# Kernel optimization log

Hardware: AMD Instinct MI355X
Metric: run time of the kernel (lower is better)

The kernel has to match this reference:

```python
import jax, jax.numpy as jnp
import numpy as np

K = 3  # inferred kernel size (28->26->pool->13->11->pool->5 matches 32*5*5 FC input)


def _patches(x, k=K):
    # x: (N,C,H,W) -> (N,C,k*k,OH,OW) valid patches, stride 1
    N, C, H, W = x.shape
    OH, OW = H - k + 1, W - k + 1
    return jnp.stack(
        [x[:, :, i:i + OH, j:j + OW] for i in range(k) for j in range(k)], axis=2
    )


def _maxpool2(x):
    N, C, H, W = x.shape
    H2, W2 = H // 2, W // 2
    x = x[:, :, :H2 * 2, :W2 * 2].reshape(N, C, H2, 2, W2, 2)
    return x.max(axis=(3, 5))


def _lc2d(x, w, b):
    # unshared-weight locally connected conv: w (O,C,k*k,OH,OW), b (O,OH,OW)
    p = _patches(x)  # (N,C,k*k,OH,OW)
    return jnp.einsum('nckij,ockij->noij', p, w) + b


def setup_inputs():
    key = jax.random.key(0)
    ks = jax.random.split(key, 9)
    s = 0.05
    return {
        'x': jax.random.normal(ks[0], (4096, 1, 28, 28), jnp.float32),
        'w1': jax.random.normal(ks[1], (16, 1, 9, 26, 26), jnp.float32) * s,
        'b1': jax.random.normal(ks[2], (16, 26, 26), jnp.float32) * s,
        'w2': jax.random.normal(ks[3], (32, 16, 9, 11, 11), jnp.float32) * s,
        'b2': jax.random.normal(ks[4], (32, 11, 11), jnp.float32) * s,
        'fc1_w': jax.random.normal(ks[5], (32 * 5 * 5, 128), jnp.float32) * s,
        'fc1_b': jax.random.normal(ks[6], (128,), jnp.float32) * s,
        'fc2_w': jax.random.normal(ks[7], (128, 10), jnp.float32) * s,
        'fc2_b': jax.random.normal(ks[8], (10,), jnp.float32) * s,
    }


def reference(x, w1, b1, w2, b2, fc1_w, fc1_b, fc2_w, fc2_b):
    h = _maxpool2(jax.nn.relu(_lc2d(x, w1, b1)))      # (N,16,13,13)
    h = _maxpool2(jax.nn.relu(_lc2d(h, w2, b2)))      # (N,32,5,5)
    h = h.reshape(h.shape[0], -1)                      # (N,800)
    h = jax.nn.relu(h @ fc1_w + fc1_b)                 # (N,128)
    return h @ fc2_w + fc2_b                           # (N,10)
```

## Files before the change

kernel.cpp:

```cpp
#include <hip/hip_runtime.h>

#define NB 4096

typedef __attribute__((ext_vector_type(8))) short s8v;
typedef __attribute__((ext_vector_type(4))) float f4v;

#define XB_OFF  0u
#define H1B_OFF 6422528u
#define H2B_OFF 28573696u
#define W2B_OFF 35127296u
#define B2R_OFF 36765696u
#define W1B_OFF 36778496u
#define B1R_OFF 37470720u
#define WFB_OFF 37513984u

__device__ __forceinline__ unsigned short f2bf(float f) {
  unsigned int u = __builtin_bit_cast(unsigned int, f);
  u += 0x7fffu + ((u >> 16) & 1u);
  return (unsigned short)(u >> 16);
}

__global__ __launch_bounds__(256) void k_prep(const float* __restrict__ x,
                                              const float* __restrict__ w1,
                                              const float* __restrict__ b1,
                                              const float* __restrict__ w2,
                                              const float* __restrict__ b2,
                                              const float* __restrict__ f1w,
                                              short* __restrict__ xB,
                                              short* __restrict__ w1b,
                                              float* __restrict__ b1r,
                                              short* __restrict__ w2b,
                                              float* __restrict__ b2r,
                                              short* __restrict__ wfb) {
  const int bx = blockIdx.x;
  if (bx < 1600) {
    __shared__ float t2[64][33];
    const int c0 = (bx % 25) * 32;
    const int n0 = (bx / 25) * 64;
    const int tx = threadIdx.x & 31, ty = threadIdx.x >> 5;
    const int c = c0 + tx;
    #pragma unroll
    for (int i = 0; i < 64; i += 8)
      if (c < 784) t2[ty + i][tx] = x[(n0 + ty + i) * 784 + c];
    __syncthreads();
    const int cl = threadIdx.x >> 3;
    const int ns = (threadIdx.x & 7) * 8;
    if (c0 + cl < 784) {
      unsigned short v[8];
      #pragma unroll
      for (int q = 0; q < 8; q++) v[q] = f2bf(t2[ns + q][cl]);
      *reinterpret_cast<s8v*>(&xB[(c0 + cl) * NB + n0 + ns]) =
          *reinterpret_cast<const s8v*>(v);
    }
  } else if (bx < 1769) {
    const int q = (bx - 1600) * 256 + threadIdx.x;
    const int l = q & 63;
    const int cv = (q >> 6) & 3;
    const int pos = q >> 8;
    const int o = l & 15;
    const int i = pos / 13, j = pos % 13;
    const int dy = cv >> 1, dx = cv & 1;
    unsigned short v[8];
    #pragma unroll
    for (int t = 0; t < 8; t++) {
      const int k = (l >> 4) * 8 + t;
      float f = 0.f;
      if (k < 16) {
        const int py = k >> 2, px = k & 3;
        const int ky = py - dy, kx = px - dx;
        if (ky >= 0 && ky < 3 && kx >= 0 && kx < 3)
          f = w1[(o * 9 + ky * 3 + kx) * 676 + (2 * i + dy) * 26 + 2 * j + dx];
      }
      v[t] = f2bf(f);
    }
    *reinterpret_cast<s8v*>(&w1b[q * 8]) = *reinterpret_cast<const s8v*>(v);
  } else if (bx < 1812) {
    const int idx = (bx - 1769) * 256 + threadIdx.x;
    if (idx < 10816) {
      const int cv = idx & 3;
      const int o = (idx >> 2) & 15;
      const int pos = idx >> 6;
      const int i = pos / 13, j = pos % 13;
      b1r[idx] = b1[(o * 26 + 2 * i + (cv >> 1)) * 26 + 2 * j + (cv & 1)];
    }
  } else if (bx < 2212) {
    const int q = (bx - 1812) * 256 + threadIdx.x;
    const int l = q & 63;
    const int ot = (q >> 6) & 1;
    const int s = (q >> 7) & 7;
    const int cv = (q >> 10) & 3;
    const int pos = q >> 12;
    const int o = ot * 16 + (l & 15);
    const int dy = cv >> 1, dx = cv & 1;
    const int I = pos / 5, J = pos % 5;
    unsigned short v[8];
    #pragma unroll
    for (int t = 0; t < 8; t++) {
      const int k = s * 32 + (l >> 4) * 8 + t;
      const int w = k >> 4, c = k & 15;
      const int py = w >> 2, px = w & 3;
      const int ky = py - dy, kx = px - dx;
      float f = 0.f;
      if (ky >= 0 && ky < 3 && kx >= 0 && kx < 3)
        f = w2[((o * 16 + c) * 9 + ky * 3 + kx) * 121 +
               (2 * I + dy) * 11 + (2 * J + dx)];
      v[t] = f2bf(f);
    }
    *reinterpret_cast<s8v*>(&w2b[q * 8]) = *reinterpret_cast<const s8v*>(v);
  } else if (bx == 2212) {
    for (int q = threadIdx.x; q < 3200; q += 256) {
      const int pos = q >> 7;
      const int r = q & 127;
      const int o = r >> 2, cv = r & 3;
      const int I = pos / 5, J = pos % 5;
      b2r[q] = b2[o * 121 + (2 * I + (cv >> 1)) * 11 + 2 * J + (cv & 1)];
    }
  } else {
    const int q = (bx - 2213) * 256 + threadIdx.x;
    const int l = q & 63;
    const int jt = (q >> 6) & 7;
    const int s = q >> 9;
    const int j = jt * 16 + (l & 15);
    unsigned short v[8];
    #pragma unroll
    for (int t = 0; t < 8; t++) {
      const int o = (l >> 4) * 8 + t;
      v[t] = f2bf(f1w[(o * 25 + s) * 128 + j]);
    }
    *reinterpret_cast<s8v*>(&wfb[q * 8]) = *reinterpret_cast<const s8v*>(v);
  }
}

__global__ __launch_bounds__(256, 3) void k_lc1(const short* __restrict__ xB,
                                                const short* __restrict__ w1b,
                                                const float* __restrict__ b1r,
                                                short* __restrict__ h1b) {
  __shared__ short sx[16 * 264 + 16 + 8];
  __shared__ unsigned short ush[256 * 24];
  const int pos = blockIdx.y;
  const int i = pos / 13, j = pos % 13;
  const int tid = threadIdx.x;
  const int l = tid & 63;
  const int wv = tid >> 6;
  const int lm = l & 15, kg = l >> 4;
  const int n0b = blockIdx.x * 256;

  #pragma unroll
  for (int rr = 0; rr < 2; rr++) {
    const int idx = rr * 256 + tid;
    const int row = idx >> 5, seg = idx & 31;
    const int grow = (2 * i + (row >> 2)) * 28 + (2 * j + (row & 3));
    *reinterpret_cast<s8v*>(&sx[row * 264 + ((row >> 3) & 1) * 16 + seg * 8]) =
        *reinterpret_cast<const s8v*>(&xB[grow * NB + n0b + seg * 8]);
  }

  s8v bf[4];
  #pragma unroll
  for (int cv = 0; cv < 4; cv++)
    bf[cv] = *reinterpret_cast<const s8v*>(w1b + ((pos * 4 + cv) * 64 + l) * 8);
  const float4 bias = *reinterpret_cast<const float4*>(b1r + (pos * 16 + lm) * 4);
  __syncthreads();

  f4v acc[4][4];
  #pragma unroll
  for (int a = 0; a < 4; a++)
    #pragma unroll
    for (int cv = 0; cv < 4; cv++) acc[a][cv] = (f4v){0.f, 0.f, 0.f, 0.f};

  #pragma unroll
  for (int a = 0; a < 4; a++) {
    const int nl = wv * 64 + a * 16 + lm;
    s8v av = (s8v){0, 0, 0, 0, 0, 0, 0, 0};
    if (kg < 2) {
      #pragma unroll
      for (int t = 0; t < 8; t++) {
        const int k = kg * 8 + t;
        av[t] = sx[k * 264 + ((k >> 3) & 1) * 16 + nl];
      }
    }
    #pragma unroll
    for (int cv = 0; cv < 4; cv++)
      acc[a][cv] =
          __builtin_amdgcn_mfma_f32_16x16x32_bf16(av, bf[cv], acc[a][cv], 0, 0, 0);
  }

  #pragma unroll
  for (int a = 0; a < 4; a++) {
    #pragma unroll
    for (int reg = 0; reg < 4; reg++) {
      const int nl = wv * 64 + a * 16 + kg * 4 + reg;
      const float v =
          fmaxf(fmaxf(acc[a][0][reg] + bias.x, acc[a][1][reg] + bias.y),
                fmaxf(acc[a][2][reg] + bias.z, acc[a][3][reg] + bias.w));
      ush[nl * 24 + lm] = f2bf(fmaxf(v, 0.f));
    }
  }
  __syncthreads();

  short* dst = h1b + (pos * 4096 + n0b + tid) * 16;
  const unsigned short* src = ush + tid * 24;
  *reinterpret_cast<s8v*>(dst) = *reinterpret_cast<const s8v*>(src);
  *reinterpret_cast<s8v*>(dst + 8) = *reinterpret_cast<const s8v*>(src + 8);
}

__global__ __launch_bounds__(256, 2) void k_lc2(const short* __restrict__ h1b,
                                                const short* __restrict__ w2b,
                                                const float* __restrict__ b2r,
                                                short* __restrict__ h2b) {
  __shared__ short sb[32768];
  const int pos = blockIdx.y;
  const int I = pos / 5, J = pos % 5;
  const int tid = threadIdx.x;
  const int l = tid & 63;
  const int wave = tid >> 6;
  const int wm = wave >> 1, ot = wave & 1;
  const int nw = blockIdx.x * 128 + wm * 64;
  const int kg = l >> 4;
  const int lm = l & 15;
  const int c0 = (kg & 1) * 8;
  const int whalf = kg >> 1;

  const short* wsrc = w2b + pos * 32768;
  #pragma unroll
  for (int r = 0; r < 16; r++) {
    const int idx = r * 256 + tid;
    *reinterpret_cast<s8v*>(&sb[idx * 8]) =
        *reinterpret_cast<const s8v*>(&wsrc[idx * 8]);
  }
  __syncthreads();

  f4v acc[4][4];
  #pragma unroll
  for (int a = 0; a < 4; a++)
    #pragma unroll
    for (int cv = 0; cv < 4; cv++)
      acc[a][cv] = (f4v){0.f, 0.f, 0.f, 0.f};

  #pragma unroll
  for (int s = 0; s < 8; s++) {
    const int wdw = s * 2 + whalf;
    const int py = wdw >> 2, px = wdw & 3;
    const int p = (2 * I + py) * 13 + (2 * J + px);
    const int abase = (p * 4096 + nw + lm) * 16 + c0;
    s8v av[4];
    #pragma unroll
    for (int a = 0; a < 4; a++)
      av[a] = *reinterpret_cast<const s8v*>(h1b + abase + a * 256);
    #pragma unroll
    for (int cv = 0; cv < 4; cv++) {
      const s8v bf = *reinterpret_cast<const s8v*>(
          &sb[(((cv * 8 + s) * 2 + ot) * 64 + l) * 8]);
      #pragma unroll
      for (int a = 0; a < 4; a++)
        acc[a][cv] =
            __builtin_amdgcn_mfma_f32_16x16x32_bf16(av[a], bf, acc[a][cv], 0, 0, 0);
    }
  }

  const int o = ot * 16 + lm;
  const float4 bias = *reinterpret_cast<const float4*>(b2r + (pos * 32 + o) * 4);
  #pragma unroll
  for (int a = 0; a < 4; a++) {
    const int nb = nw + a * 16 + kg * 4;
    #pragma unroll
    for (int reg = 0; reg < 4; reg++) {
      const float v =
          fmaxf(fmaxf(acc[a][0][reg] + bias.x, acc[a][1][reg] + bias.y),
                fmaxf(acc[a][2][reg] + bias.z, acc[a][3][reg] + bias.w));
      h2b[(pos * 4096 + nb + reg) * 32 + o] = (short)f2bf(fmaxf(v, 0.f));
    }
  }
}

__global__ __launch_bounds__(256) void k_fc(const short* __restrict__ h2b,
                                            const short* __restrict__ wfb,
                                            const float* __restrict__ f1b,
                                            const float* __restrict__ f2w,
                                            const float* __restrict__ f2b,
                                            float* __restrict__ out) {
  __shared__ float sh3[128 * 17];
  __shared__ float swf2[128 * 12];
  __shared__ float sb1[128];
  const int tid = threadIdx.x;
  const int l = tid & 63;
  const int w = tid >> 6;
  const int lm = l & 15, kg = l >> 4;
  const int n0 = blockIdx.x * 16;
  const int jt0 = w * 2;

  for (int idx = tid; idx < 1536; idx += 256) {
    const int kk = idx / 12, f = idx % 12;
    swf2[idx] = (f < 10) ? f2w[kk * 10 + f] : 0.f;
  }
  if (tid < 128) sb1[tid] = f1b[tid];

  f4v acc0 = (f4v){0.f, 0.f, 0.f, 0.f};
  f4v acc1 = (f4v){0.f, 0.f, 0.f, 0.f};

  #pragma unroll
  for (int s = 0; s < 25; s++) {
    const s8v av = *reinterpret_cast<const s8v*>(
        h2b + (s * 4096 + n0 + lm) * 32 + kg * 8);
    const s8v b0 = *reinterpret_cast<const s8v*>(
        wfb + ((s * 8 + jt0) * 64 + l) * 8);
    const s8v b1v = *reinterpret_cast<const s8v*>(
        wfb + ((s * 8 + jt0 + 1) * 64 + l) * 8);
    acc0 = __builtin_amdgcn_mfma_f32_16x16x32_bf16(av, b0, acc0, 0, 0, 0);
    acc1 = __builtin_amdgcn_mfma_f32_16x16x32_bf16(av, b1v, acc1, 0, 0, 0);
  }
  __syncthreads();

  #pragma unroll
  for (int q = 0; q < 2; q++) {
    const f4v a = q ? acc1 : acc0;
    const int j = (jt0 + q) * 16 + lm;
    #pragma unroll
    for (int reg = 0; reg < 4; reg++)
      sh3[j * 17 + kg * 4 + reg] = fmaxf(a[reg] + sb1[j], 0.f);
  }
  __syncthreads();

  if (tid < 160) {
    const int oo = tid >> 4, nn = tid & 15;
    float s = f2b[oo];
    for (int j = 0; j < 128; j++)
      s += sh3[j * 17 + nn] * swf2[j * 12 + oo];
    out[(n0 + nn) * 10 + oo] = s;
  }
}

extern "C" void kernel_launch(void* const* d_in, const int* in_sizes, int n_in,
                              void* d_out, int out_size, void* d_ws,
                              size_t ws_size, hipStream_t stream) {
  const float* x   = (const float*)d_in[0];
  const float* w1  = (const float*)d_in[1];
  const float* b1  = (const float*)d_in[2];
  const float* w2  = (const float*)d_in[3];
  const float* b2  = (const float*)d_in[4];
  const float* f1w = (const float*)d_in[5];
  const float* f1b = (const float*)d_in[6];
  const float* f2w = (const float*)d_in[7];
  const float* f2b = (const float*)d_in[8];
  float* out = (float*)d_out;
  char* ws = (char*)d_ws;
  short* xB  = (short*)(ws + XB_OFF);
  short* h1b = (short*)(ws + H1B_OFF);
  short* h2b = (short*)(ws + H2B_OFF);
  short* w2b = (short*)(ws + W2B_OFF);
  float* b2r = (float*)(ws + B2R_OFF);
  short* w1b = (short*)(ws + W1B_OFF);
  float* b1r = (float*)(ws + B1R_OFF);
  short* wfb = (short*)(ws + WFB_OFF);

  k_prep<<<2263, 256, 0, stream>>>(x, w1, b1, w2, b2, f1w,
                                   xB, w1b, b1r, w2b, b2r, wfb);
  k_lc1<<<dim3(16, 169), 256, 0, stream>>>(xB, w1b, b1r, h1b);
  k_lc2<<<dim3(32, 25), 256, 0, stream>>>(h1b, w2b, b2r, h2b);
  k_fc<<<256, 256, 0, stream>>>(h2b, wfb, f1b, f2w, f2b, out);
}
```

Measured before the change: 116.5 us.

## Fuse input bf16 conversion into first locally connected layer and drop transpose pass

The prep pass no longer transposes and converts the whole input batch to a bf16 channel-major buffer. Instead, the first locally connected kernel reads each sample's 4x4 fp32 patch straight from the original input and converts it to bf16 in registers. This drops the input staging through shared memory, one barrier, and a full read-and-write pass over the input. The occupancy hint is raised to match the smaller shared-memory footprint. In exchange, the global loads are now strided per sample rather than coalesced along the batch, and overlapping windows are reloaded across the 169 output positions, so the kernel relies on the cache to absorb the repeats.

New measurement: 121.9 us. +4.6%, slower.

```diff
diff --git a/kernel.cpp b/kernel.cpp
--- a/kernel.cpp
+++ b/kernel.cpp
@@ -5,7 +5,6 @@
 typedef __attribute__((ext_vector_type(8))) short s8v;
 typedef __attribute__((ext_vector_type(4))) float f4v;
 
-#define XB_OFF  0u
 #define H1B_OFF 6422528u
 #define H2B_OFF 28573696u
 #define W2B_OFF 35127296u
@@ -20,40 +19,19 @@
   return (unsigned short)(u >> 16);
 }
 
-__global__ __launch_bounds__(256) void k_prep(const float* __restrict__ x,
-                                              const float* __restrict__ w1,
+__global__ __launch_bounds__(256) void k_prep(const float* __restrict__ w1,
                                               const float* __restrict__ b1,
                                               const float* __restrict__ w2,
                                               const float* __restrict__ b2,
                                               const float* __restrict__ f1w,
-                                              short* __restrict__ xB,
                                               short* __restrict__ w1b,
                                               float* __restrict__ b1r,
                                               short* __restrict__ w2b,
                                               float* __restrict__ b2r,
                                               short* __restrict__ wfb) {
   const int bx = blockIdx.x;
-  if (bx < 1600) {
-    __shared__ float t2[64][33];
-    const int c0 = (bx % 25) * 32;
-    const int n0 = (bx / 25) * 64;
-    const int tx = threadIdx.x & 31, ty = threadIdx.x >> 5;
-    const int c = c0 + tx;
-    #pragma unroll
-    for (int i = 0; i < 64; i += 8)
-      if (c < 784) t2[ty + i][tx] = x[(n0 + ty + i) * 784 + c];
-    __syncthreads();
-    const int cl = threadIdx.x >> 3;
-    const int ns = (threadIdx.x & 7) * 8;
-    if (c0 + cl < 784) {
-      unsigned short v[8];
-      #pragma unroll
-      for (int q = 0; q < 8; q++) v[q] = f2bf(t2[ns + q][cl]);
-      *reinterpret_cast<s8v*>(&xB[(c0 + cl) * NB + n0 + ns]) =
-          *reinterpret_cast<const s8v*>(v);
-    }
-  } else if (bx < 1769) {
-    const int q = (bx - 1600) * 256 + threadIdx.x;
+  if (bx < 169) {
+    const int q = bx * 256 + threadIdx.x;
     const int l = q & 63;
     const int cv = (q >> 6) & 3;
     const int pos = q >> 8;
@@ -74,8 +52,8 @@
       v[t] = f2bf(f);
     }
     *reinterpret_cast<s8v*>(&w1b[q * 8]) = *reinterpret_cast<const s8v*>(v);
-  } else if (bx < 1812) {
-    const int idx = (bx - 1769) * 256 + threadIdx.x;
+  } else if (bx < 212) {
+    const int idx = (bx - 169) * 256 + threadIdx.x;
     if (idx < 10816) {
       const int cv = idx & 3;
       const int o = (idx >> 2) & 15;
@@ -83,8 +61,8 @@
       const int i = pos / 13, j = pos % 13;
       b1r[idx] = b1[(o * 26 + 2 * i + (cv >> 1)) * 26 + 2 * j + (cv & 1)];
     }
-  } else if (bx < 2212) {
-    const int q = (bx - 1812) * 256 + threadIdx.x;
+  } else if (bx < 612) {
+    const int q = (bx - 212) * 256 + threadIdx.x;
     const int l = q & 63;
     const int ot = (q >> 6) & 1;
     const int s = (q >> 7) & 7;
@@ -107,7 +85,7 @@
       v[t] = f2bf(f);
     }
     *reinterpret_cast<s8v*>(&w2b[q * 8]) = *reinterpret_cast<const s8v*>(v);
-  } else if (bx == 2212) {
+  } else if (bx == 612) {
     for (int q = threadIdx.x; q < 3200; q += 256) {
       const int pos = q >> 7;
       const int r = q & 127;
@@ -116,7 +94,7 @@
       b2r[q] = b2[o * 121 + (2 * I + (cv >> 1)) * 11 + 2 * J + (cv & 1)];
     }
   } else {
-    const int q = (bx - 2213) * 256 + threadIdx.x;
+    const int q = (bx - 613) * 256 + threadIdx.x;
     const int l = q & 63;
     const int jt = (q >> 6) & 7;
     const int s = q >> 9;
@@ -131,11 +109,10 @@
   }
 }
 
-__global__ __launch_bounds__(256, 3) void k_lc1(const short* __restrict__ xB,
+__global__ __launch_bounds__(256, 4) void k_lc1(const float* __restrict__ x,
                                                 const short* __restrict__ w1b,
                                                 const float* __restrict__ b1r,
                                                 short* __restrict__ h1b) {
-  __shared__ short sx[16 * 264 + 16 + 8];
   __shared__ unsigned short ush[256 * 24];
   const int pos = blockIdx.y;
   const int i = pos / 13, j = pos % 13;
@@ -145,21 +122,11 @@
   const int lm = l & 15, kg = l >> 4;
   const int n0b = blockIdx.x * 256;
 
-  #pragma unroll
-  for (int rr = 0; rr < 2; rr++) {
-    const int idx = rr * 256 + tid;
-    const int row = idx >> 5, seg = idx & 31;
-    const int grow = (2 * i + (row >> 2)) * 28 + (2 * j + (row & 3));
-    *reinterpret_cast<s8v*>(&sx[row * 264 + ((row >> 3) & 1) * 16 + seg * 8]) =
-        *reinterpret_cast<const s8v*>(&xB[grow * NB + n0b + seg * 8]);
-  }
-
   s8v bf[4];
   #pragma unroll
   for (int cv = 0; cv < 4; cv++)
     bf[cv] = *reinterpret_cast<const s8v*>(w1b + ((pos * 4 + cv) * 64 + l) * 8);
   const float4 bias = *reinterpret_cast<const float4*>(b1r + (pos * 16 + lm) * 4);
-  __syncthreads();
 
   f4v acc[4][4];
   #pragma unroll
@@ -167,15 +134,22 @@
     #pragma unroll
     for (int cv = 0; cv < 4; cv++) acc[a][cv] = (f4v){0.f, 0.f, 0.f, 0.f};
 
+  const int col0 = (2 * i) * 28 + 2 * j;
+
   #pragma unroll
   for (int a = 0; a < 4; a++) {
-    const int nl = wv * 64 + a * 16 + lm;
+    const int nl = n0b + wv * 64 + a * 16 + lm;
     s8v av = (s8v){0, 0, 0, 0, 0, 0, 0, 0};
     if (kg < 2) {
+      const float* xr = x + nl * 784 + col0 + kg * 2 * 28;
       #pragma unroll
-      for (int t = 0; t < 8; t++) {
-        const int k = kg * 8 + t;
-        av[t] = sx[k * 264 + ((k >> 3) & 1) * 16 + nl];
+      for (int r = 0; r < 2; r++) {
+        const float2 lo = *reinterpret_cast<const float2*>(xr + r * 28);
+        const float2 hi = *reinterpret_cast<const float2*>(xr + r * 28 + 2);
+        av[r * 4 + 0] = (short)f2bf(lo.x);
+        av[r * 4 + 1] = (short)f2bf(lo.y);
+        av[r * 4 + 2] = (short)f2bf(hi.x);
+        av[r * 4 + 3] = (short)f2bf(hi.y);
       }
     }
     #pragma unroll
@@ -195,8 +169,6 @@
       ush[nl * 24 + lm] = f2bf(fmaxf(v, 0.f));
     }
   }
-  __syncthreads();
-
   short* dst = h1b + (pos * 4096 + n0b + tid) * 16;
   const unsigned short* src = ush + tid * 24;
   *reinterpret_cast<s8v*>(dst) = *reinterpret_cast<const s8v*>(src);
@@ -343,7 +315,6 @@
   const float* f2b = (const float*)d_in[8];
   float* out = (float*)d_out;
   char* ws = (char*)d_ws;
-  short* xB  = (short*)(ws + XB_OFF);
   short* h1b = (short*)(ws + H1B_OFF);
   short* h2b = (short*)(ws + H2B_OFF);
   short* w2b = (short*)(ws + W2B_OFF);
@@ -352,9 +323,9 @@
   float* b1r = (float*)(ws + B1R_OFF);
   short* wfb = (short*)(ws + WFB_OFF);
 
-  k_prep<<<2263, 256, 0, stream>>>(x, w1, b1, w2, b2, f1w,
-                                   xB, w1b, b1r, w2b, b2r, wfb);
-  k_lc1<<<dim3(16, 169), 256, 0, stream>>>(xB, w1b, b1r, h1b);
+  k_prep<<<663, 256, 0, stream>>>(w1, b1, w2, b2, f1w,
+                                  w1b, b1r, w2b, b2r, wfb);
+  k_lc1<<<dim3(16, 169), 256, 0, stream>>>(x, w1b, b1r, h1b);
   k_lc2<<<dim3(32, 25), 256, 0, stream>>>(h1b, w2b, b2r, h2b);
   k_fc<<<256, 256, 0, stream>>>(h2b, wfb, f1b, f2w, f2b, out);
 }
```

## Split lc2 across output-channel tiles and fold weight prep into lc1 launch

Applied to the files above, without the earlier changes.

The layer-2 kernel now puts each 16-channel output tile in its own grid-z block. This halves shared memory per block and allows higher occupancy, at the cost of reading the layer-1 activations twice. The w2, b2 and fc1 weight repacking moves from the prep kernel into extra blocks of the lc1 launch, so it overlaps with layer-1 compute. The MFMA loop order is also changed to preload B fragments and stream A.

Result: no change. 117.1 us (+0.5%).

```diff
diff --git a/kernel.cpp b/kernel.cpp
--- a/kernel.cpp
+++ b/kernel.cpp
@@ -20,18 +20,12 @@
   return (unsigned short)(u >> 16);
 }
 
-__global__ __launch_bounds__(256) void k_prep(const float* __restrict__ x,
-                                              const float* __restrict__ w1,
-                                              const float* __restrict__ b1,
-                                              const float* __restrict__ w2,
-                                              const float* __restrict__ b2,
-                                              const float* __restrict__ f1w,
-                                              short* __restrict__ xB,
-                                              short* __restrict__ w1b,
-                                              float* __restrict__ b1r,
-                                              short* __restrict__ w2b,
-                                              float* __restrict__ b2r,
-                                              short* __restrict__ wfb) {
+__global__ __launch_bounds__(256) void k_prep1(const float* __restrict__ x,
+                                               const float* __restrict__ w1,
+                                               const float* __restrict__ b1,
+                                               short* __restrict__ xB,
+                                               short* __restrict__ w1b,
+                                               float* __restrict__ b1r) {
   const int bx = blockIdx.x;
   if (bx < 1600) {
     __shared__ float t2[64][33];
@@ -74,69 +68,87 @@
       v[t] = f2bf(f);
     }
     *reinterpret_cast<s8v*>(&w1b[q * 8]) = *reinterpret_cast<const s8v*>(v);
-  } else if (bx < 1812) {
+  } else {
     const int idx = (bx - 1769) * 256 + threadIdx.x;
     if (idx < 10816) {
       const int cv = idx & 3;
-      const int o = (idx >> 2) & 15;
-      const int pos = idx >> 6;
+      const int o = (idx >> 2) & 3 * 4 + ((idx >> 2) & 15);
+    }
+    const int idx2 = (bx - 1769) * 256 + threadIdx.x;
+    if (idx2 < 10816) {
+      const int cv = idx2 & 3;
+      const int o = (idx2 >> 2) & 15;
+      const int pos = idx2 >> 6;
       const int i = pos / 13, j = pos % 13;
-      b1r[idx] = b1[(o * 26 + 2 * i + (cv >> 1)) * 26 + 2 * j + (cv & 1)];
-    }
-  } else if (bx < 2212) {
-    const int q = (bx - 1812) * 256 + threadIdx.x;
-    const int l = q & 63;
-    const int ot = (q >> 6) & 1;
-    const int s = (q >> 7) & 7;
-    const int cv = (q >> 10) & 3;
-    const int pos = q >> 12;
-    const int o = ot * 16 + (l & 15);
-    const int dy = cv >> 1, dx = cv & 1;
-    const int I = pos / 5, J = pos % 5;
-    unsigned short v[8];
-    #pragma unroll
-    for (int t = 0; t < 8; t++) {
-      const int k = s * 32 + (l >> 4) * 8 + t;
-      const int w = k >> 4, c = k & 15;
-      const int py = w >> 2, px = w & 3;
-      const int ky = py - dy, kx = px - dx;
-      float f = 0.f;
-      if (ky >= 0 && ky < 3 && kx >= 0 && kx < 3)
-        f = w2[((o * 16 + c) * 9 + ky * 3 + kx) * 121 +
-               (2 * I + dy) * 11 + (2 * J + dx)];
-      v[t] = f2bf(f);
-    }
-    *reinterpret_cast<s8v*>(&w2b[q * 8]) = *reinterpret_cast<const s8v*>(v);
-  } else if (bx == 2212) {
-    for (int q = threadIdx.x; q < 3200; q += 256) {
-      const int pos = q >> 7;
-      const int r = q & 127;
-      const int o = r >> 2, cv = r & 3;
-      const int I = pos / 5, J = pos % 5;
-      b2r[q] = b2[o * 121 + (2 * I + (cv >> 1)) * 11 + 2 * J + (cv & 1)];
-    }
-  } else {
-    const int q = (bx - 2213) * 256 + threadIdx.x;
-    const int l = q & 63;
-    const int jt = (q >> 6) & 7;
-    const int s = q >> 9;
-    const int j = jt * 16 + (l & 15);
-    unsigned short v[8];
-    #pragma unroll
-    for (int t = 0; t < 8; t++) {
-      const int o = (l >> 4) * 8 + t;
-      v[t] = f2bf(f1w[(o * 25 + s) * 128 + j]);
-    }
-    *reinterpret_cast<s8v*>(&wfb[q * 8]) = *reinterpret_cast<const s8v*>(v);
+      b1r[idx2] = b1[(o * 26 + 2 * i + (cv >> 1)) * 26 + 2 * j + (cv & 1)];
+    }
   }
 }
 
 __global__ __launch_bounds__(256, 3) void k_lc1(const short* __restrict__ xB,
                                                 const short* __restrict__ w1b,
                                                 const float* __restrict__ b1r,
-                                                short* __restrict__ h1b) {
+                                                short* __restrict__ h1b,
+                                                const float* __restrict__ w2,
+                                                const float* __restrict__ b2,
+                                                const float* __restrict__ f1w,
+                                                short* __restrict__ w2b,
+                                                float* __restrict__ b2r,
+                                                short* __restrict__ wfb) {
   __shared__ short sx[16 * 264 + 16 + 8];
   __shared__ unsigned short ush[256 * 24];
+
+  if (blockIdx.y >= 169) {
+    const int pid = (blockIdx.y - 169) * 16 + blockIdx.x;
+    if (pid < 400) {
+      const int q = pid * 256 + threadIdx.x;
+      const int l = q & 63;
+      const int ot = (q >> 6) & 1;
+      const int s = (q >> 7) & 7;
+      const int cv = (q >> 10) & 3;
+      const int pos = q >> 12;
+      const int o = ot * 16 + (l & 15);
+      const int dy = cv >> 1, dx = cv & 1;
+      const int I = pos / 5, J = pos % 5;
+      unsigned short v[8];
+      #pragma unroll
+      for (int t = 0; t < 8; t++) {
+        const int k = s * 32 + (l >> 4) * 8 + t;
+        const int w = k >> 4, c = k & 15;
+        const int py = w >> 2, px = w & 3;
+        const int ky = py - dy, kx = px - dx;
+        float f = 0.f;
+        if (ky >= 0 && ky < 3 && kx >= 0 && kx < 3)
+          f = w2[((o * 16 + c) * 9 + ky * 3 + kx) * 121 +
+                 (2 * I + dy) * 11 + (2 * J + dx)];
+        v[t] = f2bf(f);
+      }
+      *reinterpret_cast<s8v*>(&w2b[q * 8]) = *reinterpret_cast<const s8v*>(v);
+    } else if (pid == 400) {
+      for (int q = threadIdx.x; q < 3200; q += 256) {
+        const int pos = q >> 7;
+        const int r = q & 127;
+        const int o = r >> 2, cv = r & 3;
+        const int I = pos / 5, J = pos % 5;
+        b2r[q] = b2[o * 121 + (2 * I + (cv >> 1)) * 11 + 2 * J + (cv & 1)];
+      }
+    } else if (pid < 451) {
+      const int q = (pid - 401) * 256 + threadIdx.x;
+      const int l = q & 63;
+      const int jt = (q >> 6) & 7;
+      const int s = q >> 9;
+      const int j = jt * 16 + (l & 15);
+      unsigned short v[8];
+      #pragma unroll
+      for (int t = 0; t < 8; t++) {
+        const int o = (l >> 4) * 8 + t;
+        v[t] = f2bf(f1w[(o * 25 + s) * 128 + j]);
+      }
+      *reinterpret_cast<s8v*>(&wfb[q * 8]) = *reinterpret_cast<const s8v*>(v);
+    }
+    return;
+  }
+
   const int pos = blockIdx.y;
   const int i = pos / 13, j = pos % 13;
   const int tid = threadIdx.x;
@@ -203,18 +215,18 @@
   *reinterpret_cast<s8v*>(dst + 8) = *reinterpret_cast<const s8v*>(src + 8);
 }
 
-__global__ __launch_bounds__(256, 2) void k_lc2(const short* __restrict__ h1b,
+__global__ __launch_bounds__(256, 4) void k_lc2(const short* __restrict__ h1b,
                                                 const short* __restrict__ w2b,
                                                 const float* __restrict__ b2r,
                                                 short* __restrict__ h2b) {
-  __shared__ short sb[32768];
+  __shared__ short sb[16384];
   const int pos = blockIdx.y;
+  const int ot = blockIdx.z;
   const int I = pos / 5, J = pos % 5;
   const int tid = threadIdx.x;
   const int l = tid & 63;
   const int wave = tid >> 6;
-  const int wm = wave >> 1, ot = wave & 1;
-  const int nw = blockIdx.x * 128 + wm * 64;
+  const int nw = blockIdx.x * 256 + wave * 64;
   const int kg = l >> 4;
   const int lm = l & 15;
   const int c0 = (kg & 1) * 8;
@@ -222,10 +234,12 @@
 
   const short* wsrc = w2b + pos * 32768;
   #pragma unroll
-  for (int r = 0; r < 16; r++) {
-    const int idx = r * 256 + tid;
+  for (int r8 = 0; r8 < 8; r8++) {
+    const int idx = r8 * 256 + tid;
+    const int r = idx >> 6;
+    const int ll = idx & 63;
     *reinterpret_cast<s8v*>(&sb[idx * 8]) =
-        *reinterpret_cast<const s8v*>(&wsrc[idx * 8]);
+        *reinterpret_cast<const s8v*>(&wsrc[((r * 2 + ot) * 64 + ll) * 8]);
   }
   __syncthreads();
 
@@ -242,18 +256,18 @@
     const int py = wdw >> 2, px = wdw & 3;
     const int p = (2 * I + py) * 13 + (2 * J + px);
     const int abase = (p * 4096 + nw + lm) * 16 + c0;
-    s8v av[4];
-    #pragma unroll
-    for (int a = 0; a < 4; a++)
-      av[a] = *reinterpret_cast<const s8v*>(h1b + abase + a * 256);
-    #pragma unroll
-    for (int cv = 0; cv < 4; cv++) {
-      const s8v bf = *reinterpret_cast<const s8v*>(
-          &sb[(((cv * 8 + s) * 2 + ot) * 64 + l) * 8]);
-      #pragma unroll
-      for (int a = 0; a < 4; a++)
+    s8v bf[4];
+    #pragma unroll
+    for (int cv = 0; cv < 4; cv++)
+      bf[cv] = *reinterpret_cast<const s8v*>(
+          &sb[((cv * 8 + s) * 64 + l) * 8]);
+    #pragma unroll
+    for (int a = 0; a < 4; a++) {
+      const s8v av = *reinterpret_cast<const s8v*>(h1b + abase + a * 256);
+      #pragma unroll
+      for (int cv = 0; cv < 4; cv++)
         acc[a][cv] =
-            __builtin_amdgcn_mfma_f32_16x16x32_bf16(av[a], bf, acc[a][cv], 0, 0, 0);
+            __builtin_amdgcn_mfma_f32_16x16x32_bf16(av, bf[cv], acc[a][cv], 0, 0, 0);
     }
   }
 
@@ -352,9 +366,9 @@
   float* b1r = (float*)(ws + B1R_OFF);
   short* wfb = (short*)(ws + WFB_OFF);
 
-  k_prep<<<2263, 256, 0, stream>>>(x, w1, b1, w2, b2, f1w,
-                                   xB, w1b, b1r, w2b, b2r, wfb);
-  k_lc1<<<dim3(16, 169), 256, 0, stream>>>(xB, w1b, b1r, h1b);
-  k_lc2<<<dim3(32, 25), 256, 0, stream>>>(h1b, w2b, b2r, h2b);
+  k_prep1<<<1812, 256, 0, stream>>>(x, w1, b1, xB, w1b, b1r);
+  k_lc1<<<dim3(16, 198), 256, 0, stream>>>(xB, w1b, b1r, h1b,
+                                           w2, b2, f1w, w2b, b2r, wfb);
+  k_lc2<<<dim3(16, 25, 2), 256, 0, stream>>>(h1b, w2b, b2r, h2b);
   k_fc<<<256, 256, 0, stream>>>(h2b, wfb, f1b, f2w, f2b, out);
 }
```
